# Kernel tuning notes

Measured on AMD Instinct MI355X. Metric: run time of the kernel, lower is better.

## Reference

```python
import jax, jax.numpy as jnp
import numpy as np
from functools import partial

N_NODES = 50000
N_EDGES = 800000
IN_F, HID_F, OUT_F = 128, 128, 64


def _linear_params(key, in_f, out_f):
    k1, k2 = jax.random.split(key)
    bound = 1.0 / np.sqrt(in_f)
    W = jax.random.uniform(k1, (out_f, in_f), jnp.float32, -bound, bound)
    b = jax.random.uniform(k2, (out_f,), jnp.float32, -bound, bound)
    return W, b


def setup_inputs() -> dict:
    key = jax.random.key(0)
    ks = jax.random.split(key, 10)
    features = jax.random.normal(ks[0], (N_NODES, IN_F), jnp.float32)
    src = jax.random.randint(ks[1], (N_EDGES,), 0, N_NODES, jnp.int32)
    dst = jax.random.randint(ks[2], (N_EDGES,), 0, N_NODES, jnp.int32)
    W1a, b1a = _linear_params(ks[3], IN_F, HID_F)
    W1b, b1b = _linear_params(ks[4], HID_F, HID_F)
    W2a, b2a = _linear_params(ks[5], HID_F, HID_F)
    W2b, b2b = _linear_params(ks[6], HID_F, HID_F)
    W3a, b3a = _linear_params(ks[7], HID_F, HID_F)
    W3b, b3b = _linear_params(ks[8], HID_F, OUT_F)
    return dict(features=features, src=src, dst=dst,
                W1a=W1a, b1a=b1a, W1b=W1b, b1b=b1b,
                W2a=W2a, b2a=b2a, W2b=W2b, b2b=b2b,
                W3a=W3a, b3a=b3a, W3b=W3b, b3b=b3b)


def _mean_agg(x, src, dst, n_nodes):
    # gather src features, segment-sum into dst, divide by in-degree (0-deg -> 0)
    summed = jax.ops.segment_sum(x[src], dst, num_segments=n_nodes)
    deg = jax.ops.segment_sum(jnp.ones((src.shape[0],), x.dtype), dst,
                              num_segments=n_nodes)
    return summed / jnp.maximum(deg, 1.0)[:, None]


def _gin_conv(x, src, dst, Wa, ba, Wb, bb):
    # DGL GINConv, aggregator 'mean', eps=0: h = MLP((1+eps)*x + mean_agg)
    h = x + _mean_agg(x, src, dst, x.shape[0])
    h = jax.nn.relu(h @ Wa.T + ba)
    return h @ Wb.T + bb


def reference(features, src, dst,
              W1a, b1a, W1b, b1b,
              W2a, b2a, W2b, b2b,
              W3a, b3a, W3b, b3b):
    x = jax.nn.relu(_gin_conv(features, src, dst, W1a, b1a, W1b, b1b))
    x = jax.nn.relu(_gin_conv(x, src, dst, W2a, b2a, W2b, b2b))
    x = jax.nn.relu(x @ W3a.T + b3a)
    return x @ W3b.T + b3b
```

## Files before the change

kernel.cpp:

```cpp
#include <hip/hip_runtime.h>
#include <hip/hip_fp16.h>

#define N_NODES 50000
#define N_EDGES 800000

typedef __attribute__((ext_vector_type(8))) short bf16x8;
typedef __attribute__((ext_vector_type(4))) float f32x4;

#define OFF_BUFA   0UL
#define OFF_T16    25600000UL
#define OFF_CNT    38400000UL
#define OFF_W      38600064UL
#define OFF_CSR    38960512UL

#define NB_EDGE 3125
#define NB_W    352
#define NB_FEAT 6250

__device__ __forceinline__ unsigned short bf16_rne(float f) {
  unsigned u = __float_as_uint(f);
  unsigned r = (u + 0x7FFFu + ((u >> 16) & 1u)) >> 16;
  return (unsigned short)r;
}

__device__ __forceinline__ int swz(int row, int b) {
  return (row * 256 + b) ^ ((row & 7) << 4);
}

__global__ __launch_bounds__(256)
void prep_kernel(const int* __restrict__ src, const int* __restrict__ dst,
                 int* __restrict__ cnt, int* __restrict__ csr,
                 const float* __restrict__ W1a, const float* __restrict__ W1b,
                 const float* __restrict__ W2a, const float* __restrict__ W2b,
                 const float* __restrict__ W3a, const float* __restrict__ W3b,
                 unsigned short* __restrict__ pool,
                 const float* __restrict__ feat, __half* __restrict__ t16) {
  const int b = blockIdx.x;
  const int tid = threadIdx.x;
  if (b < NB_EDGE) {
    int i = b * 256 + tid;
    int d = dst[i];
    int pos = atomicAdd(&cnt[d], 1);
    if (pos < 64) csr[(d << 6) + pos] = src[i];
  } else if (b < NB_EDGE + NB_W) {
    int i = (b - NB_EDGE) * 256 + tid;
    const float* s;
    int base, local, msize;
    if (i < 16384)      { s = W1a; base = 0;      local = i;          msize = 16384; }
    else if (i < 32768) { s = W1b; base = 32768;  local = i - 16384;  msize = 16384; }
    else if (i < 49152) { s = W2a; base = 65536;  local = i - 32768;  msize = 16384; }
    else if (i < 65536) { s = W2b; base = 98304;  local = i - 49152;  msize = 16384; }
    else if (i < 81920) { s = W3a; base = 131072; local = i - 65536;  msize = 16384; }
    else                { s = W3b; base = 163840; local = i - 81920;  msize = 8192;  }
    float f = s[local];
    unsigned short hi = bf16_rne(f);
    float fh = __uint_as_float((unsigned)hi << 16);
    pool[base + local] = hi;
    pool[base + msize + local] = bf16_rne(f - fh);
  } else {
    int i = (b - NB_EDGE - NB_W) * 1024 + tid * 4;
    float4 v = *reinterpret_cast<const float4*>(feat + i);
    ushort4 h;
    h.x = __half_as_ushort(__float2half_rn(v.x));
    h.y = __half_as_ushort(__float2half_rn(v.y));
    h.z = __half_as_ushort(__float2half_rn(v.z));
    h.w = __half_as_ushort(__float2half_rn(v.w));
    *reinterpret_cast<ushort4*>((unsigned short*)t16 + i) = h;
  }
}

template <bool SELF32>
__global__ __launch_bounds__(256)
void agg_kernel(const __half* __restrict__ t16, const float* __restrict__ xself,
                const int* __restrict__ csr, const int* __restrict__ cnt,
                float* __restrict__ out) {
  int node = blockIdx.x * 4 + (threadIdx.x >> 6);
  if (node >= N_NODES) return;
  const int lane = threadIdx.x & 63;
  int deg = cnt[node];
  int dloop = min(deg, 64);
  int beg = node << 6;
  float inv = 1.0f / fmaxf((float)deg, 1.0f);

  float s0 = 0.f, s1 = 0.f, t0 = 0.f, t1 = 0.f;
  float u0 = 0.f, u1 = 0.f, v0 = 0.f, v1 = 0.f;
  int e = 0;
  for (; e + 3 < dloop; e += 4) {
    int i0 = csr[beg + e], i1 = csr[beg + e + 1], i2 = csr[beg + e + 2], i3 = csr[beg + e + 3];
    float2 a = __half22float2(*reinterpret_cast<const __half2*>(t16 + (size_t)i0 * 128 + lane * 2));
    float2 b = __half22float2(*reinterpret_cast<const __half2*>(t16 + (size_t)i1 * 128 + lane * 2));
    float2 c = __half22float2(*reinterpret_cast<const __half2*>(t16 + (size_t)i2 * 128 + lane * 2));
    float2 d = __half22float2(*reinterpret_cast<const __half2*>(t16 + (size_t)i3 * 128 + lane * 2));
    s0 += a.x; s1 += a.y; t0 += b.x; t1 += b.y;
    u0 += c.x; u1 += c.y; v0 += d.x; v1 += d.y;
  }
  for (; e < dloop; ++e) {
    int i0 = csr[beg + e];
    float2 a = __half22float2(*reinterpret_cast<const __half2*>(t16 + (size_t)i0 * 128 + lane * 2));
    s0 += a.x; s1 += a.y;
  }
  float2 sm = make_float2(s0 + t0 + u0 + v0, s1 + t1 + u1 + v1);
  float2 xv;
  if (SELF32) {
    xv = *reinterpret_cast<const float2*>(xself + (size_t)node * 128 + lane * 2);
  } else {
    xv = __half22float2(*reinterpret_cast<const __half2*>(t16 + (size_t)node * 128 + lane * 2));
  }
  float2 o = make_float2(fmaf(sm.x, inv, xv.x), fmaf(sm.y, inv, xv.y));
  *reinterpret_cast<float2*>(out + (size_t)node * 128 + lane * 2) = o;
}

__device__ __forceinline__ void stage_x(const float* __restrict__ X, int m0, int tid,
                                        char* ahi, char* alo, int M) {
  #pragma unroll
  for (int it = 0; it < 8; ++it) {
    int f = tid + it * 256;
    int row = f >> 5, c = f & 31;
    float4 v = make_float4(0.f, 0.f, 0.f, 0.f);
    if (m0 + row < M)
      v = *reinterpret_cast<const float4*>(X + (size_t)(m0 + row) * 128 + c * 4);
    ushort4 hi, lo;
    float fh;
    hi.x = bf16_rne(v.x); fh = __uint_as_float((unsigned)hi.x << 16); lo.x = bf16_rne(v.x - fh);
    hi.y = bf16_rne(v.y); fh = __uint_as_float((unsigned)hi.y << 16); lo.y = bf16_rne(v.y - fh);
    hi.z = bf16_rne(v.z); fh = __uint_as_float((unsigned)hi.z << 16); lo.z = bf16_rne(v.z - fh);
    hi.w = bf16_rne(v.w); fh = __uint_as_float((unsigned)hi.w << 16); lo.w = bf16_rne(v.w - fh);
    int bo = swz(row, c * 8);
    *reinterpret_cast<ushort4*>(ahi + bo) = hi;
    *reinterpret_cast<ushort4*>(alo + bo) = lo;
  }
}

template <int NB>
__device__ __forceinline__ void load_bfrag(const unsigned short* __restrict__ Wh,
                                           const unsigned short* __restrict__ Wl,
                                           int w, int lrow, int lg,
                                           bf16x8 (&bh)[NB][4], bf16x8 (&bl)[NB][4]) {
  #pragma unroll
  for (int nb = 0; nb < NB; ++nb) {
    int col = w * (16 * NB) + nb * 16 + lrow;
    #pragma unroll
    for (int kk = 0; kk < 4; ++kk) {
      int idx = col * 128 + kk * 32 + lg * 8;
      bh[nb][kk] = *reinterpret_cast<const bf16x8*>(Wh + idx);
      bl[nb][kk] = *reinterpret_cast<const bf16x8*>(Wl + idx);
    }
  }
}

template <int NB>
__device__ __forceinline__ void gemm_lds(const char* ahi, const char* alo, int lrow, int lg,
                                         const bf16x8 (&bh)[NB][4], const bf16x8 (&bl)[NB][4],
                                         f32x4 (&acc)[4][NB]) {
  #pragma unroll
  for (int i = 0; i < 4; ++i)
    #pragma unroll
    for (int nb = 0; nb < NB; ++nb) acc[i][nb] = (f32x4){0.f, 0.f, 0.f, 0.f};
  #pragma unroll
  for (int i = 0; i < 4; ++i) {
    #pragma unroll
    for (int kk = 0; kk < 4; ++kk) {
      int bo = swz(i * 16 + lrow, kk * 64 + lg * 16);
      bf16x8 ah = *reinterpret_cast<const bf16x8*>(ahi + bo);
      bf16x8 al = *reinterpret_cast<const bf16x8*>(alo + bo);
      #pragma unroll
      for (int nb = 0; nb < NB; ++nb) {
        acc[i][nb] = __builtin_amdgcn_mfma_f32_16x16x32_bf16(ah, bh[nb][kk], acc[i][nb], 0, 0, 0);
        acc[i][nb] = __builtin_amdgcn_mfma_f32_16x16x32_bf16(al, bh[nb][kk], acc[i][nb], 0, 0, 0);
        acc[i][nb] = __builtin_amdgcn_mfma_f32_16x16x32_bf16(ah, bl[nb][kk], acc[i][nb], 0, 0, 0);
      }
    }
  }
}

__device__ __forceinline__ void store_h(char* ahi, char* alo, const float* __restrict__ bias,
                                        int w, int lrow, int lg, f32x4 (&acc)[4][2]) {
  #pragma unroll
  for (int i = 0; i < 4; ++i) {
    #pragma unroll
    for (int nb = 0; nb < 2; ++nb) {
      int col = w * 32 + nb * 16 + lrow;
      float b = bias[col];
      #pragma unroll
      for (int r = 0; r < 4; ++r) {
        float v = fmaxf(acc[i][nb][r] + b, 0.f);
        int row = i * 16 + lg * 4 + r;
        unsigned short h = bf16_rne(v);
        float fh = __uint_as_float((unsigned)h << 16);
        unsigned short l2 = bf16_rne(v - fh);
        int bo = swz(row, col * 2);
        *reinterpret_cast<unsigned short*>(ahi + bo) = h;
        *reinterpret_cast<unsigned short*>(alo + bo) = l2;
      }
    }
  }
}

__global__ __launch_bounds__(256)
void mlp1_kernel(const float* __restrict__ X, const unsigned short* __restrict__ p,
                 const float* __restrict__ b1a, const float* __restrict__ b1b,
                 __half* __restrict__ Y, int M) {
  __shared__ unsigned short Ahi[64 * 128];
  __shared__ unsigned short Alo[64 * 128];
  char* ahi = (char*)Ahi;
  char* alo = (char*)Alo;
  const int tid = threadIdx.x;
  const int w = tid >> 6, l = tid & 63;
  const int lrow = l & 15, lg = l >> 4;
  const int m0 = blockIdx.x * 64;

  stage_x(X, m0, tid, ahi, alo, M);
  __syncthreads();

  f32x4 acc[4][2];
  {
    bf16x8 bh[2][4], bl[2][4];
    load_bfrag<2>(p + 0, p + 16384, w, lrow, lg, bh, bl);
    gemm_lds<2>(ahi, alo, lrow, lg, bh, bl, acc);
  }
  __syncthreads();
  {
    bf16x8 bh[2][4], bl[2][4];
    load_bfrag<2>(p + 32768, p + 49152, w, lrow, lg, bh, bl);
    store_h(ahi, alo, b1a, w, lrow, lg, acc);
    __syncthreads();
    gemm_lds<2>(ahi, alo, lrow, lg, bh, bl, acc);
  }
  #pragma unroll
  for (int i = 0; i < 4; ++i) {
    #pragma unroll
    for (int nb = 0; nb < 2; ++nb) {
      int col = w * 32 + nb * 16 + lrow;
      float b = b1b[col];
      #pragma unroll
      for (int r = 0; r < 4; ++r) {
        float v = fmaxf(acc[i][nb][r] + b, 0.f);
        int row = m0 + i * 16 + lg * 4 + r;
        if (row < M) Y[(size_t)row * 128 + col] = __float2half_rn(v);
      }
    }
  }
}

__global__ __launch_bounds__(256)
void mlp2head_kernel(const float* __restrict__ X, const unsigned short* __restrict__ p,
                     const float* __restrict__ b2a, const float* __restrict__ b2b,
                     const float* __restrict__ b3a, const float* __restrict__ b3b,
                     float* __restrict__ Y, int M) {
  __shared__ unsigned short Ahi[64 * 128];
  __shared__ unsigned short Alo[64 * 128];
  char* ahi = (char*)Ahi;
  char* alo = (char*)Alo;
  const int tid = threadIdx.x;
  const int w = tid >> 6, l = tid & 63;
  const int lrow = l & 15, lg = l >> 4;
  const int m0 = blockIdx.x * 64;

  stage_x(X, m0, tid, ahi, alo, M);
  __syncthreads();

  f32x4 acc[4][2];
  {
    bf16x8 bh[2][4], bl[2][4];
    load_bfrag<2>(p + 65536, p + 81920, w, lrow, lg, bh, bl);
    gemm_lds<2>(ahi, alo, lrow, lg, bh, bl, acc);
  }
  __syncthreads();
  {
    bf16x8 bh[2][4], bl[2][4];
    load_bfrag<2>(p + 98304, p + 114688, w, lrow, lg, bh, bl);
    store_h(ahi, alo, b2a, w, lrow, lg, acc);
    __syncthreads();
    gemm_lds<2>(ahi, alo, lrow, lg, bh, bl, acc);
  }
  __syncthreads();
  {
    bf16x8 bh[2][4], bl[2][4];
    load_bfrag<2>(p + 131072, p + 147456, w, lrow, lg, bh, bl);
    store_h(ahi, alo, b2b, w, lrow, lg, acc);
    __syncthreads();
    gemm_lds<2>(ahi, alo, lrow, lg, bh, bl, acc);
  }
  __syncthreads();
  f32x4 acc1[4][1];
  {
    bf16x8 bh[1][4], bl[1][4];
    load_bfrag<1>(p + 163840, p + 172032, w, lrow, lg, bh, bl);
    store_h(ahi, alo, b3a, w, lrow, lg, acc);
    __syncthreads();
    gemm_lds<1>(ahi, alo, lrow, lg, bh, bl, acc1);
  }
  #pragma unroll
  for (int i = 0; i < 4; ++i) {
    int col = w * 16 + lrow;
    float b = b3b[col];
    #pragma unroll
    for (int r = 0; r < 4; ++r) {
      float v = acc1[i][0][r] + b;
      int row = m0 + i * 16 + lg * 4 + r;
      if (row < M) Y[(size_t)row * 64 + col] = v;
    }
  }
}

extern "C" void kernel_launch(void* const* d_in, const int* in_sizes, int n_in,
                              void* d_out, int out_size, void* d_ws, size_t ws_size,
                              hipStream_t stream) {
  const float* feat = (const float*)d_in[0];
  const int*   esrc = (const int*)d_in[1];
  const int*   edst = (const int*)d_in[2];
  const float* W1a = (const float*)d_in[3];  const float* b1a = (const float*)d_in[4];
  const float* W1b = (const float*)d_in[5];  const float* b1b = (const float*)d_in[6];
  const float* W2a = (const float*)d_in[7];  const float* b2a = (const float*)d_in[8];
  const float* W2b = (const float*)d_in[9];  const float* b2b = (const float*)d_in[10];
  const float* W3a = (const float*)d_in[11]; const float* b3a = (const float*)d_in[12];
  const float* W3b = (const float*)d_in[13]; const float* b3b = (const float*)d_in[14];

  char* ws = (char*)d_ws;
  float*  bufA = (float*)(ws + OFF_BUFA);
  __half* t16  = (__half*)(ws + OFF_T16);
  int*    cnt  = (int*)(ws + OFF_CNT);
  unsigned short* p = (unsigned short*)(ws + OFF_W);
  int*    csr  = (int*)(ws + OFF_CSR);

  hipMemsetAsync(cnt, 0, 200000, stream);

  prep_kernel<<<NB_EDGE + NB_W + NB_FEAT, 256, 0, stream>>>(
      esrc, edst, cnt, csr, W1a, W1b, W2a, W2b, W3a, W3b, p, feat, t16);

  const int AB = (N_NODES + 3) / 4;
  const int GB = (N_NODES + 63) / 64;

  agg_kernel<true><<<AB, 256, 0, stream>>>(t16, feat, csr, cnt, bufA);
  mlp1_kernel<<<GB, 256, 0, stream>>>(bufA, p, b1a, b1b, t16, N_NODES);

  agg_kernel<false><<<AB, 256, 0, stream>>>(t16, feat, csr, cnt, bufA);
  mlp2head_kernel<<<GB, 256, 0, stream>>>(bufA, p, b2a, b2b, b3a, b3b,
                                          (float*)d_out, N_NODES);
}
```

Measured before the change: 212.4 us.

## Switch MLP GEMMs to fp16 activations with split fp16 weights; compact CSR to u16

Replaces the bf16 hi/lo split of both activations and weights (three MFMAs per tile) with a single fp16 activation tile and fp16 weights split into a high part and a scaled low residual (two MFMAs into separate accumulators, merged with a 1/2048 scale). This halves LDS staging and removes the activation-splitting arithmetic. The CSR neighbour list is stored as 16-bit indices and read four at a time. Biases are packed into the weight pool, and the GEMM kernels gain an occupancy hint of two blocks per CU. The trade-off is lower activation precision from fp16 rounding. The u16 CSR indices silently truncate node ids at 65535, which only works because this graph has 50000 nodes.

```diff
diff --git a/kernel.cpp b/kernel.cpp
--- a/kernel.cpp
+++ b/kernel.cpp
@@ -4,61 +4,74 @@
 #define N_NODES 50000
 #define N_EDGES 800000
 
-typedef __attribute__((ext_vector_type(8))) short bf16x8;
+typedef __attribute__((ext_vector_type(8))) short s16x8;
+typedef _Float16 f16x8 __attribute__((ext_vector_type(8)));
 typedef __attribute__((ext_vector_type(4))) float f32x4;
 
 #define OFF_BUFA   0UL
 #define OFF_T16    25600000UL
 #define OFF_CNT    38400000UL
 #define OFF_W      38600064UL
-#define OFF_CSR    38960512UL
+#define OFF_CSR    38963328UL
 
 #define NB_EDGE 3125
-#define NB_W    352
+#define NB_WB   355
 #define NB_FEAT 6250
 
-__device__ __forceinline__ unsigned short bf16_rne(float f) {
-  unsigned u = __float_as_uint(f);
-  unsigned r = (u + 0x7FFFu + ((u >> 16) & 1u)) >> 16;
-  return (unsigned short)r;
-}
+#define INV2048 4.8828125e-4f
 
 __device__ __forceinline__ int swz(int row, int b) {
   return (row * 256 + b) ^ ((row & 7) << 4);
 }
 
 __global__ __launch_bounds__(256)
-void prep_kernel(const int* __restrict__ src, const int* __restrict__ dst,
-                 int* __restrict__ cnt, int* __restrict__ csr,
-                 const float* __restrict__ W1a, const float* __restrict__ W1b,
-                 const float* __restrict__ W2a, const float* __restrict__ W2b,
-                 const float* __restrict__ W3a, const float* __restrict__ W3b,
+void prep_kernel(const int* __restrict__ esrc, const int* __restrict__ edst,
+                 int* __restrict__ cnt, unsigned short* __restrict__ csr,
+                 const float* __restrict__ W1a, const float* __restrict__ b1a,
+                 const float* __restrict__ W1b, const float* __restrict__ b1b,
+                 const float* __restrict__ W2a, const float* __restrict__ b2a,
+                 const float* __restrict__ W2b, const float* __restrict__ b2b,
+                 const float* __restrict__ W3a, const float* __restrict__ b3a,
+                 const float* __restrict__ W3b, const float* __restrict__ b3b,
                  unsigned short* __restrict__ pool,
                  const float* __restrict__ feat, __half* __restrict__ t16) {
   const int b = blockIdx.x;
   const int tid = threadIdx.x;
   if (b < NB_EDGE) {
     int i = b * 256 + tid;
-    int d = dst[i];
+    int d = edst[i];
     int pos = atomicAdd(&cnt[d], 1);
-    if (pos < 64) csr[(d << 6) + pos] = src[i];
-  } else if (b < NB_EDGE + NB_W) {
+    if (pos < 64) csr[(d << 6) + pos] = (unsigned short)esrc[i];
+  } else if (b < NB_EDGE + NB_WB) {
     int i = (b - NB_EDGE) * 256 + tid;
-    const float* s;
-    int base, local, msize;
-    if (i < 16384)      { s = W1a; base = 0;      local = i;          msize = 16384; }
-    else if (i < 32768) { s = W1b; base = 32768;  local = i - 16384;  msize = 16384; }
-    else if (i < 49152) { s = W2a; base = 65536;  local = i - 32768;  msize = 16384; }
-    else if (i < 65536) { s = W2b; base = 98304;  local = i - 49152;  msize = 16384; }
-    else if (i < 81920) { s = W3a; base = 131072; local = i - 65536;  msize = 16384; }
-    else                { s = W3b; base = 163840; local = i - 81920;  msize = 8192;  }
-    float f = s[local];
-    unsigned short hi = bf16_rne(f);
-    float fh = __uint_as_float((unsigned)hi << 16);
-    pool[base + local] = hi;
-    pool[base + msize + local] = bf16_rne(f - fh);
+    if (i < 90112) {
+      const float* s;
+      int base, local, msize;
+      if (i < 16384)      { s = W1a; base = 0;      local = i;          msize = 16384; }
+      else if (i < 32768) { s = W1b; base = 32768;  local = i - 16384;  msize = 16384; }
+      else if (i < 49152) { s = W2a; base = 65536;  local = i - 32768;  msize = 16384; }
+      else if (i < 65536) { s = W2b; base = 98304;  local = i - 49152;  msize = 16384; }
+      else if (i < 81920) { s = W3a; base = 131072; local = i - 65536;  msize = 16384; }
+      else                { s = W3b; base = 163840; local = i - 81920;  msize = 8192;  }
+      float f = s[local];
+      __half h = __float2half_rn(f);
+      float fh = __half2float(h);
+      __half l = __float2half_rn((f - fh) * 2048.0f);
+      pool[base + local] = __half_as_ushort(h);
+      pool[base + msize + local] = __half_as_ushort(l);
+    } else if (i < 90816) {
+      int j = i - 90112;
+      const float* s; int o;
+      if (j < 128)      { s = b1a; o = j; }
+      else if (j < 256) { s = b1b; o = j - 128; }
+      else if (j < 384) { s = b2a; o = j - 256; }
+      else if (j < 512) { s = b2b; o = j - 384; }
+      else if (j < 640) { s = b3a; o = j - 512; }
+      else              { s = b3b; o = j - 640; }
+      ((float*)(pool + 180224))[j] = s[o];
+    }
   } else {
-    int i = (b - NB_EDGE - NB_W) * 1024 + tid * 4;
+    int i = (b - NB_EDGE - NB_WB) * 1024 + tid * 4;
     float4 v = *reinterpret_cast<const float4*>(feat + i);
     ushort4 h;
     h.x = __half_as_ushort(__float2half_rn(v.x));
@@ -72,7 +85,7 @@
 template <bool SELF32>
 __global__ __launch_bounds__(256)
 void agg_kernel(const __half* __restrict__ t16, const float* __restrict__ xself,
-                const int* __restrict__ csr, const int* __restrict__ cnt,
+                const unsigned short* __restrict__ csr, const int* __restrict__ cnt,
                 float* __restrict__ out) {
   int node = blockIdx.x * 4 + (threadIdx.x >> 6);
   if (node >= N_NODES) return;
@@ -86,11 +99,11 @@
   float u0 = 0.f, u1 = 0.f, v0 = 0.f, v1 = 0.f;
   int e = 0;
   for (; e + 3 < dloop; e += 4) {
-    int i0 = csr[beg + e], i1 = csr[beg + e + 1], i2 = csr[beg + e + 2], i3 = csr[beg + e + 3];
-    float2 a = __half22float2(*reinterpret_cast<const __half2*>(t16 + (size_t)i0 * 128 + lane * 2));
-    float2 b = __half22float2(*reinterpret_cast<const __half2*>(t16 + (size_t)i1 * 128 + lane * 2));
-    float2 c = __half22float2(*reinterpret_cast<const __half2*>(t16 + (size_t)i2 * 128 + lane * 2));
-    float2 d = __half22float2(*reinterpret_cast<const __half2*>(t16 + (size_t)i3 * 128 + lane * 2));
+    ushort4 q = *reinterpret_cast<const ushort4*>(csr + beg + e);
+    float2 a = __half22float2(*reinterpret_cast<const __half2*>(t16 + (size_t)q.x * 128 + lane * 2));
+    float2 b = __half22float2(*reinterpret_cast<const __half2*>(t16 + (size_t)q.y * 128 + lane * 2));
+    float2 c = __half22float2(*reinterpret_cast<const __half2*>(t16 + (size_t)q.z * 128 + lane * 2));
+    float2 d = __half22float2(*reinterpret_cast<const __half2*>(t16 + (size_t)q.w * 128 + lane * 2));
     s0 += a.x; s1 += a.y; t0 += b.x; t1 += b.y;
     u0 += c.x; u1 += c.y; v0 += d.x; v1 += d.y;
   }
@@ -111,70 +124,65 @@
 }
 
 __device__ __forceinline__ void stage_x(const float* __restrict__ X, int m0, int tid,
-                                        char* ahi, char* alo, int M) {
-  #pragma unroll
-  for (int it = 0; it < 8; ++it) {
+                                        char* a16, int M) {
+  #pragma unroll
+  for (int it = 0; it < 4; ++it) {
     int f = tid + it * 256;
-    int row = f >> 5, c = f & 31;
-    float4 v = make_float4(0.f, 0.f, 0.f, 0.f);
-    if (m0 + row < M)
-      v = *reinterpret_cast<const float4*>(X + (size_t)(m0 + row) * 128 + c * 4);
-    ushort4 hi, lo;
-    float fh;
-    hi.x = bf16_rne(v.x); fh = __uint_as_float((unsigned)hi.x << 16); lo.x = bf16_rne(v.x - fh);
-    hi.y = bf16_rne(v.y); fh = __uint_as_float((unsigned)hi.y << 16); lo.y = bf16_rne(v.y - fh);
-    hi.z = bf16_rne(v.z); fh = __uint_as_float((unsigned)hi.z << 16); lo.z = bf16_rne(v.z - fh);
-    hi.w = bf16_rne(v.w); fh = __uint_as_float((unsigned)hi.w << 16); lo.w = bf16_rne(v.w - fh);
-    int bo = swz(row, c * 8);
-    *reinterpret_cast<ushort4*>(ahi + bo) = hi;
-    *reinterpret_cast<ushort4*>(alo + bo) = lo;
+    int row = f >> 4, c8 = (f & 15) * 8;
+    float4 v0 = make_float4(0.f, 0.f, 0.f, 0.f), v1 = v0;
+    if (m0 + row < M) {
+      const float* xp = X + (size_t)(m0 + row) * 128 + c8;
+      v0 = *reinterpret_cast<const float4*>(xp);
+      v1 = *reinterpret_cast<const float4*>(xp + 4);
+    }
+    f16x8 hv;
+    hv[0] = (_Float16)v0.x; hv[1] = (_Float16)v0.y; hv[2] = (_Float16)v0.z; hv[3] = (_Float16)v0.w;
+    hv[4] = (_Float16)v1.x; hv[5] = (_Float16)v1.y; hv[6] = (_Float16)v1.z; hv[7] = (_Float16)v1.w;
+    *reinterpret_cast<f16x8*>(a16 + swz(row, c8 * 2)) = hv;
   }
 }
 
 template <int NB>
-__device__ __forceinline__ void load_bfrag(const unsigned short* __restrict__ Wh,
-                                           const unsigned short* __restrict__ Wl,
+__device__ __forceinline__ void gemm_stage(const char* a16,
+                                           const unsigned short* __restrict__ wh,
+                                           const unsigned short* __restrict__ wl,
                                            int w, int lrow, int lg,
-                                           bf16x8 (&bh)[NB][4], bf16x8 (&bl)[NB][4]) {
+                                           f32x4 (&acch)[4][NB], f32x4 (&accl)[4][NB]) {
+  f16x8 bh[NB][4], bl[NB][4];
   #pragma unroll
   for (int nb = 0; nb < NB; ++nb) {
     int col = w * (16 * NB) + nb * 16 + lrow;
     #pragma unroll
     for (int kk = 0; kk < 4; ++kk) {
       int idx = col * 128 + kk * 32 + lg * 8;
-      bh[nb][kk] = *reinterpret_cast<const bf16x8*>(Wh + idx);
-      bl[nb][kk] = *reinterpret_cast<const bf16x8*>(Wl + idx);
-    }
-  }
-}
-
-template <int NB>
-__device__ __forceinline__ void gemm_lds(const char* ahi, const char* alo, int lrow, int lg,
-                                         const bf16x8 (&bh)[NB][4], const bf16x8 (&bl)[NB][4],
-                                         f32x4 (&acc)[4][NB]) {
+      bh[nb][kk] = *reinterpret_cast<const f16x8*>(wh + idx);
+      bl[nb][kk] = *reinterpret_cast<const f16x8*>(wl + idx);
+    }
+  }
   #pragma unroll
   for (int i = 0; i < 4; ++i)
     #pragma unroll
-    for (int nb = 0; nb < NB; ++nb) acc[i][nb] = (f32x4){0.f, 0.f, 0.f, 0.f};
-  #pragma unroll
-  for (int i = 0; i < 4; ++i) {
-    #pragma unroll
-    for (int kk = 0; kk < 4; ++kk) {
-      int bo = swz(i * 16 + lrow, kk * 64 + lg * 16);
-      bf16x8 ah = *reinterpret_cast<const bf16x8*>(ahi + bo);
-      bf16x8 al = *reinterpret_cast<const bf16x8*>(alo + bo);
+    for (int nb = 0; nb < NB; ++nb) {
+      acch[i][nb] = (f32x4){0.f, 0.f, 0.f, 0.f};
+      accl[i][nb] = (f32x4){0.f, 0.f, 0.f, 0.f};
+    }
+  #pragma unroll
+  for (int kk = 0; kk < 4; ++kk) {
+    #pragma unroll
+    for (int i = 0; i < 4; ++i) {
+      f16x8 a = *reinterpret_cast<const f16x8*>(a16 + swz(i * 16 + lrow, kk * 64 + lg * 16));
       #pragma unroll
       for (int nb = 0; nb < NB; ++nb) {
-        acc[i][nb] = __builtin_amdgcn_mfma_f32_16x16x32_bf16(ah, bh[nb][kk], acc[i][nb], 0, 0, 0);
-        acc[i][nb] = __builtin_amdgcn_mfma_f32_16x16x32_bf16(al, bh[nb][kk], acc[i][nb], 0, 0, 0);
-        acc[i][nb] = __builtin_amdgcn_mfma_f32_16x16x32_bf16(ah, bl[nb][kk], acc[i][nb], 0, 0, 0);
+        acch[i][nb] = __builtin_amdgcn_mfma_f32_16x16x32_f16(a, bh[nb][kk], acch[i][nb], 0, 0, 0);
+        accl[i][nb] = __builtin_amdgcn_mfma_f32_16x16x32_f16(a, bl[nb][kk], accl[i][nb], 0, 0, 0);
       }
     }
   }
 }
 
-__device__ __forceinline__ void store_h(char* ahi, char* alo, const float* __restrict__ bias,
-                                        int w, int lrow, int lg, f32x4 (&acc)[4][2]) {
+__device__ __forceinline__ void store_h(char* a16, const float* __restrict__ bias,
+                                        int w, int lrow, int lg,
+                                        f32x4 (&acch)[4][2], f32x4 (&accl)[4][2]) {
   #pragma unroll
   for (int i = 0; i < 4; ++i) {
     #pragma unroll
@@ -183,58 +191,45 @@
       float b = bias[col];
       #pragma unroll
       for (int r = 0; r < 4; ++r) {
-        float v = fmaxf(acc[i][nb][r] + b, 0.f);
+        float v = fmaxf(fmaf(accl[i][nb][r], INV2048, acch[i][nb][r]) + b, 0.f);
         int row = i * 16 + lg * 4 + r;
-        unsigned short h = bf16_rne(v);
-        float fh = __uint_as_float((unsigned)h << 16);
-        unsigned short l2 = bf16_rne(v - fh);
-        int bo = swz(row, col * 2);
-        *reinterpret_cast<unsigned short*>(ahi + bo) = h;
-        *reinterpret_cast<unsigned short*>(alo + bo) = l2;
+        *reinterpret_cast<unsigned short*>(a16 + swz(row, col * 2)) =
+            __half_as_ushort(__float2half_rn(v));
       }
     }
   }
 }
 
-__global__ __launch_bounds__(256)
+__global__ __launch_bounds__(256, 2)
 void mlp1_kernel(const float* __restrict__ X, const unsigned short* __restrict__ p,
-                 const float* __restrict__ b1a, const float* __restrict__ b1b,
                  __half* __restrict__ Y, int M) {
-  __shared__ unsigned short Ahi[64 * 128];
-  __shared__ unsigned short Alo[64 * 128];
-  char* ahi = (char*)Ahi;
-  char* alo = (char*)Alo;
+  __shared__ __align__(16) unsigned short A16[64 * 128];
+  char* a16 = (char*)A16;
+  const float* biases = (const float*)(p + 180224);
   const int tid = threadIdx.x;
   const int w = tid >> 6, l = tid & 63;
   const int lrow = l & 15, lg = l >> 4;
   const int m0 = blockIdx.x * 64;
 
-  stage_x(X, m0, tid, ahi, alo, M);
+  stage_x(X, m0, tid, a16, M);
   __syncthreads();
 
-  f32x4 acc[4][2];
-  {
-    bf16x8 bh[2][4], bl[2][4];
-    load_bfrag<2>(p + 0, p + 16384, w, lrow, lg, bh, bl);
-    gemm_lds<2>(ahi, alo, lrow, lg, bh, bl, acc);
-  }
+  f32x4 acch[4][2], accl[4][2];
+  gemm_stage<2>(a16, p + 0, p + 16384, w, lrow, lg, acch, accl);
   __syncthreads();
-  {
-    bf16x8 bh[2][4], bl[2][4];
-    load_bfrag<2>(p + 32768, p + 49152, w, lrow, lg, bh, bl);
-    store_h(ahi, alo, b1a, w, lrow, lg, acc);
-    __syncthreads();
-    gemm_lds<2>(ahi, alo, lrow, lg, bh, bl, acc);
-  }
+  store_h(a16, biases + 0, w, lrow, lg, acch, accl);
+  __syncthreads();
+  gemm_stage<2>(a16, p + 32768, p + 49152, w, lrow, lg, acch, accl);
+
   #pragma unroll
   for (int i = 0; i < 4; ++i) {
     #pragma unroll
     for (int nb = 0; nb < 2; ++nb) {
       int col = w * 32 + nb * 16 + lrow;
-      float b = b1b[col];
+      float b = biases[128 + col];
       #pragma unroll
       for (int r = 0; r < 4; ++r) {
-        float v = fmaxf(acc[i][nb][r] + b, 0.f);
+        float v = fmaxf(fmaf(accl[i][nb][r], INV2048, acch[i][nb][r]) + b, 0.f);
         int row = m0 + i * 16 + lg * 4 + r;
         if (row < M) Y[(size_t)row * 128 + col] = __float2half_rn(v);
       }
@@ -242,61 +237,40 @@
   }
 }
 
-__global__ __launch_bounds__(256)
+__global__ __launch_bounds__(256, 2)
 void mlp2head_kernel(const float* __restrict__ X, const unsigned short* __restrict__ p,
-                     const float* __restrict__ b2a, const float* __restrict__ b2b,
-                     const float* __restrict__ b3a, const float* __restrict__ b3b,
                      float* __restrict__ Y, int M) {
-  __shared__ unsigned short Ahi[64 * 128];
-  __shared__ unsigned short Alo[64 * 128];
-  char* ahi = (char*)Ahi;
-  char* alo = (char*)Alo;
+  __shared__ __align__(16) unsigned short A16[64 * 128];
+  char* a16 = (char*)A16;
+  const float* biases = (const float*)(p + 180224);
   const int tid = threadIdx.x;
   const int w = tid >> 6, l = tid & 63;
   const int lrow = l & 15, lg = l >> 4;
   const int m0 = blockIdx.x * 64;
 
-  stage_x(X, m0, tid, ahi, alo, M);
+  stage_x(X, m0, tid, a16, M);
   __syncthreads();
 
-  f32x4 acc[4][2];
-  {
-    bf16x8 bh[2][4], bl[2][4];
-    load_bfrag<2>(p + 65536, p + 81920, w, lrow, lg, bh, bl);
-    gemm_lds<2>(ahi, alo, lrow, lg, bh, bl, acc);
-  }
-  __syncthreads();
-  {
-    bf16x8 bh[2][4], bl[2][4];
-    load_bfrag<2>(p + 98304, p + 114688, w, lrow, lg, bh, bl);
-    store_h(ahi, alo, b2a, w, lrow, lg, acc);
+  #pragma unroll 1
+  for (int s = 0; s < 3; ++s) {
+    const unsigned short* wh = p + 65536 + s * 32768;
+    const unsigned short* wl = wh + 16384;
+    f32x4 acch[4][2], accl[4][2];
+    gemm_stage<2>(a16, wh, wl, w, lrow, lg, acch, accl);
     __syncthreads();
-    gemm_lds<2>(ahi, alo, lrow, lg, bh, bl, acc);
-  }
-  __syncthreads();
-  {
-    bf16x8 bh[2][4], bl[2][4];
-    load_bfrag<2>(p + 131072, p + 147456, w, lrow, lg, bh, bl);
-    store_h(ahi, alo, b2b, w, lrow, lg, acc);
+    store_h(a16, biases + 256 + s * 128, w, lrow, lg, acch, accl);
     __syncthreads();
-    gemm_lds<2>(ahi, alo, lrow, lg, bh, bl, acc);
-  }
-  __syncthreads();
-  f32x4 acc1[4][1];
-  {
-    bf16x8 bh[1][4], bl[1][4];
-    load_bfrag<1>(p + 163840, p + 172032, w, lrow, lg, bh, bl);
-    store_h(ahi, alo, b3a, w, lrow, lg, acc);
-    __syncthreads();
-    gemm_lds<1>(ahi, alo, lrow, lg, bh, bl, acc1);
-  }
+  }
+
+  f32x4 acch[4][1], accl[4][1];
+  gemm_stage<1>(a16, p + 163840, p + 172032, w, lrow, lg, acch, accl);
   #pragma unroll
   for (int i = 0; i < 4; ++i) {
     int col = w * 16 + lrow;
-    float b = b3b[col];
+    float b = biases[640 + col];
     #pragma unroll
     for (int r = 0; r < 4; ++r) {
-      float v = acc1[i][0][r] + b;
+      float v = fmaf(accl[i][0][r], INV2048, acch[i][0][r]) + b;
       int row = m0 + i * 16 + lg * 4 + r;
       if (row < M) Y[(size_t)row * 64 + col] = v;
     }
@@ -320,21 +294,22 @@
   float*  bufA = (float*)(ws + OFF_BUFA);
   __half* t16  = (__half*)(ws + OFF_T16);
   int*    cnt  = (int*)(ws + OFF_CNT);
-  unsigned short* p = (unsigned short*)(ws + OFF_W);
-  int*    csr  = (int*)(ws + OFF_CSR);
+  unsigned short* p   = (unsigned short*)(ws + OFF_W);
+  unsigned short* csr = (unsigned short*)(ws + OFF_CSR);
 
   hipMemsetAsync(cnt, 0, 200000, stream);
 
-  prep_kernel<<<NB_EDGE + NB_W + NB_FEAT, 256, 0, stream>>>(
-      esrc, edst, cnt, csr, W1a, W1b, W2a, W2b, W3a, W3b, p, feat, t16);
+  prep_kernel<<<NB_EDGE + NB_WB + NB_FEAT, 256, 0, stream>>>(
+      esrc, edst, cnt, csr,
+      W1a, b1a, W1b, b1b, W2a, b2a, W2b, b2b, W3a, b3a, W3b, b3b,
+      p, feat, t16);
 
   const int AB = (N_NODES + 3) / 4;
   const int GB = (N_NODES + 63) / 64;
 
   agg_kernel<true><<<AB, 256, 0, stream>>>(t16, feat, csr, cnt, bufA);
-  mlp1_kernel<<<GB, 256, 0, stream>>>(bufA, p, b1a, b1b, t16, N_NODES);
+  mlp1_kernel<<<GB, 256, 0, stream>>>(bufA, p, t16, N_NODES);
 
   agg_kernel<false><<<AB, 256, 0, stream>>>(t16, feat, csr, cnt, bufA);
-  mlp2head_kernel<<<GB, 256, 0, stream>>>(bufA, p, b2a, b2b, b3a, b3b,
-                                          (float*)d_out, N_NODES);
-}
+  mlp2head_kernel<<<GB, 256, 0, stream>>>(bufA, p, (float*)d_out, N_NODES);
+}
```

Result: no change. 209.5 us (-1.4%).
